# Kernel optimization log

Measured on AMD Instinct MI355X. Metric: run time of the kernel, lower is better.

The kernel has to match this reference:

```python
import jax, jax.numpy as jnp
import numpy as np

B, N, S, D, H = 64, 4096, 8, 256, 512
ITERS = 3
EPS = 1e-8      # slot-attention renormalize epsilon
LN_EPS = 1e-5   # torch LayerNorm default


def _ln(x, g, b):
    m = jnp.mean(x, -1, keepdims=True)
    v = jnp.mean((x - m) ** 2, -1, keepdims=True)
    return (x - m) * jax.lax.rsqrt(v + LN_EPS) * g + b


def setup_inputs() -> dict:
    key = jax.random.key(0)
    ks = jax.random.split(key, 12)

    def xav(k, shape):
        s = (6.0 / (shape[-2] + shape[-1])) ** 0.5
        return jax.random.uniform(k, shape, jnp.float32, -s, s)

    gru_s = 1.0 / (D ** 0.5)
    return {
        "inputs": jax.random.normal(ks[0], (B, N, D), jnp.float32),
        "init_noise": jax.random.normal(ks[1], (B, S, D), jnp.float32),
        "slots_mu": xav(ks[2], (1, 1, D)),
        "slots_log_sigma": xav(ks[3], (1, 1, D)),
        "ln_in_g": jnp.ones(D), "ln_in_b": jnp.zeros(D),
        "ln_slots_g": jnp.ones(D), "ln_slots_b": jnp.zeros(D),
        "ln_mlp_g": jnp.ones(D), "ln_mlp_b": jnp.zeros(D),
        "Wq": xav(ks[4], (D, D)),
        "Wk": xav(ks[5], (D, D)),
        "Wv": xav(ks[6], (D, D)),
        "W_ih": jax.random.uniform(ks[7], (3 * D, D), jnp.float32, -gru_s, gru_s),
        "W_hh": jax.random.uniform(ks[8], (3 * D, D), jnp.float32, -gru_s, gru_s),
        "b_ih": jnp.zeros(3 * D), "b_hh": jnp.zeros(3 * D),
        "W1": xav(ks[9], (H, D)), "b1": jnp.zeros(H),
        "W2": xav(ks[10], (D, H)), "b2": jnp.zeros(D),
    }


def reference(inputs, init_noise, slots_mu, slots_log_sigma,
              ln_in_g, ln_in_b, ln_slots_g, ln_slots_b, ln_mlp_g, ln_mlp_b,
              Wq, Wk, Wv, W_ih, W_hh, b_ih, b_hh, W1, b1, W2, b2):
    x = _ln(inputs, ln_in_g, ln_in_b)               # (B,N,D)
    k = jnp.einsum('bnd,ed->bne', x, Wk)             # (B,N,D)
    v = jnp.einsum('bnd,ed->bne', x, Wv)             # (B,N,D)
    slots = slots_mu + jnp.exp(slots_log_sigma) * init_noise  # (B,S,D)
    scale = D ** (-0.5)
    for _ in range(ITERS):
        prev = slots
        s = _ln(slots, ln_slots_g, ln_slots_b)
        q = jnp.einsum('bsd,ed->bse', s, Wq) * scale
        logits = jnp.einsum('bse,bne->bsn', q, k)    # (B,S,N)
        attn = jax.nn.softmax(logits, -1) + EPS
        attn = attn / jnp.sum(attn, -1, keepdims=True)
        upd = jnp.einsum('bsn,bne->bse', attn, v)    # (B,S,D)
        # GRUCell (torch semantics)
        gx = jnp.einsum('bsd,ed->bse', upd, W_ih) + b_ih
        gh = jnp.einsum('bsd,ed->bse', prev, W_hh) + b_hh
        xr, xz, xn = jnp.split(gx, 3, -1)
        hr, hz, hn = jnp.split(gh, 3, -1)
        r = jax.nn.sigmoid(xr + hr)
        z = jax.nn.sigmoid(xz + hz)
        n = jnp.tanh(xn + r * hn)
        slots = (1.0 - z) * n + z * prev
        # residual MLP
        m = _ln(slots, ln_mlp_g, ln_mlp_b)
        h1 = jax.nn.relu(jnp.einsum('bsd,hd->bsh', m, W1) + b1)
        slots = slots + jnp.einsum('bsh,dh->bsd', h1, W2) + b2
    return slots
```

## Files before the change

kernel.cpp:

```cpp
#include <hip/hip_runtime.h>

#define BB 64
#define NN 4096
#define SS 8
#define DD 256
#define HH 512
#define NCH 8
#define CHK 512
#define LSP 516

typedef __attribute__((ext_vector_type(4))) float f32x4;
typedef __attribute__((ext_vector_type(8))) short short8;
typedef __attribute__((ext_vector_type(8))) __bf16 bf16x8;

static __device__ __forceinline__ f32x4 MFMA(short8 a, short8 b, f32x4 c){
  return __builtin_amdgcn_mfma_f32_16x16x32_bf16(
      __builtin_bit_cast(bf16x8, a), __builtin_bit_cast(bf16x8, b), c, 0, 0, 0);
}

static __device__ __forceinline__ unsigned short f2bf(float f){
  unsigned int x = __builtin_bit_cast(unsigned int, f);
  x += 0x7FFFu + ((x >> 16) & 1u);
  return (unsigned short)(x >> 16);
}

static __device__ __forceinline__ unsigned int pk2(float a, float b){
  return (unsigned int)f2bf(a) | ((unsigned int)f2bf(b) << 16);
}

struct PackDesc {
  const float* src[7];
  unsigned short* dst[7];
  int ET[7];
  int K[7];
  int blkStart[8];
};

__global__ void pack_all_kernel(PackDesc pd){
  int blk = blockIdx.x;
  int seg = 0;
  #pragma unroll
  for(int i = 1; i < 7; ++i) if(blk >= pd.blkStart[i]) seg = i;
  int tid = (blk - pd.blkStart[seg]) * 256 + threadIdx.x;
  int ET = pd.ET[seg], K = pd.K[seg];
  if(tid >= ET * 16 * K) return;
  int i    = tid & 7;
  int lane = (tid >> 3) & 63;
  int rest = tid >> 9;
  int et = rest % ET;
  int kk = rest / ET;
  int row = et * 16 + (lane & 15);
  int col = kk * 32 + ((lane >> 4) << 3) + i;
  pd.dst[seg][tid] = f2bf(pd.src[seg][(size_t)row * K + col]);
}

__global__ __launch_bounds__(256, 2) void proj_kernel(
    const float* __restrict__ inp, const float* __restrict__ g, const float* __restrict__ bta,
    const short8* __restrict__ wkp, const short8* __restrict__ wvp,
    unsigned short* __restrict__ kout, unsigned short* __restrict__ vT)
{
  __shared__ unsigned short xs[64 * 256];
  __shared__ unsigned short vstage[4][1024];
  const int t = threadIdx.x, w = t >> 6, l = t & 63;
  const size_t row0 = (size_t)blockIdx.x * 64;
  const int b = (int)(row0 >> 12);
  const int n_base = (int)(row0 & 4095);
  const int li = l & 15, lg = l >> 4;

  {
    float4 gg[4], bb[4];
    #pragma unroll
    for(int q = 0; q < 4; ++q){
      gg[q] = ((const float4*)g)[li + q * 16];
      bb[q] = ((const float4*)bta)[li + q * 16];
    }
    #pragma unroll
    for(int rr = 0; rr < 4; ++rr){
      int r = w * 16 + rr * 4 + lg;
      const float4* rp = (const float4*)(inp + (row0 + r) * DD);
      float4 x[4];
      #pragma unroll
      for(int q = 0; q < 4; ++q) x[q] = rp[li + q * 16];
      float s1 = 0.f, s2 = 0.f;
      #pragma unroll
      for(int q = 0; q < 4; ++q){
        s1 += x[q].x + x[q].y + x[q].z + x[q].w;
        s2 += x[q].x*x[q].x + x[q].y*x[q].y + x[q].z*x[q].z + x[q].w*x[q].w;
      }
      #pragma unroll
      for(int o = 8; o >= 1; o >>= 1){ s1 += __shfl_xor(s1, o); s2 += __shfl_xor(s2, o); }
      float mean = s1 * (1.0f/256.0f);
      float inv  = rsqrtf(s2 * (1.0f/256.0f) - mean*mean + 1e-5f);
      #pragma unroll
      for(int q = 0; q < 4; ++q){
        float y0 = (x[q].x-mean)*inv*gg[q].x + bb[q].x;
        float y1 = (x[q].y-mean)*inv*gg[q].y + bb[q].y;
        float y2 = (x[q].z-mean)*inv*gg[q].z + bb[q].z;
        float y3 = (x[q].w-mean)*inv*gg[q].w + bb[q].w;
        int byte = r * 512 + ((q * 128 + li * 8) ^ ((r & 7) << 4));
        *(uint2*)((char*)xs + byte) = make_uint2(pk2(y0,y1), pk2(y2,y3));
      }
    }
  }
  __syncthreads();

  const int et0 = w * 4;
  #pragma unroll
  for(int el = 0; el < 4; ++el){
    const int et = et0 + el;
    short8 wb[8];
    #pragma unroll
    for(int kk = 0; kk < 8; ++kk) wb[kk] = wkp[((kk * 16 + et) << 6) + l];
    #pragma unroll
    for(int rg = 0; rg < 4; ++rg){
      const int r = rg * 16 + li;
      f32x4 a = (f32x4){0,0,0,0};
      #pragma unroll
      for(int kk = 0; kk < 8; ++kk){
        int ab = r * 512 + (((kk * 64) + (lg << 4)) ^ ((r & 7) << 4));
        short8 afr = *(const short8*)((const char*)xs + ab);
        a = MFMA(wb[kk], afr, a);
      }
      size_t row = row0 + rg * 16 + li;
      int colb = et * 16 + (lg << 2);
      *(uint2*)(kout + row * DD + colb) = make_uint2(pk2(a[0],a[1]), pk2(a[2],a[3]));
    }
  }
  #pragma unroll
  for(int el = 0; el < 4; ++el){
    const int et = et0 + el;
    short8 wb[8];
    #pragma unroll
    for(int kk = 0; kk < 8; ++kk) wb[kk] = wvp[((kk * 16 + et) << 6) + l];
    char* vs = (char*)&vstage[w][0];
    #pragma unroll
    for(int rg = 0; rg < 4; ++rg){
      const int r = rg * 16 + li;
      f32x4 a = (f32x4){0,0,0,0};
      #pragma unroll
      for(int kk = 0; kk < 8; ++kk){
        int ab = r * 512 + (((kk * 64) + (lg << 4)) ^ ((r & 7) << 4));
        short8 afr = *(const short8*)((const char*)xs + ab);
        a = MFMA(afr, wb[kk], a);
      }
      int nloc = rg * 16 + (lg << 2);
      int byte = li * 128 + ((nloc * 2) ^ ((li & 7) << 4));
      *(uint2*)(vs + byte) = make_uint2(pk2(a[0],a[1]), pk2(a[2],a[3]));
    }
    asm volatile("s_waitcnt lgkmcnt(0)" ::: "memory");
    #pragma unroll
    for(int u = 0; u < 2; ++u){
      int dl = u * 8 + (l >> 3);
      int byte = dl * 128 + (((l & 7) * 16) ^ ((dl & 7) << 4));
      uint4 vv = *(uint4*)(vs + byte);
      int d = et * 16 + dl;
      *(uint4*)(vT + ((size_t)(b * 256 + d) << 12) + n_base + (l & 7) * 8) = vv;
    }
    asm volatile("" ::: "memory");
  }
}

__global__ __launch_bounds__(256, 1) void init_kernel(
    const float* __restrict__ noise, const float* __restrict__ mu, const float* __restrict__ lsg,
    const float* __restrict__ lng, const float* __restrict__ lnb,
    const short8* __restrict__ wqp, float* __restrict__ slots, float* __restrict__ qbuf)
{
  const int b = blockIdx.x, t = threadIdx.x, w = t >> 6, l = t & 63;
  __shared__ float SLN[SS * DD];
  __shared__ unsigned short A1[16 * DD];
  float muv = mu[t];
  float sgv = __expf(lsg[t]);
  #pragma unroll
  for(int s = 0; s < SS; ++s){
    float v = muv + sgv * noise[(size_t)b * 2048 + s * 256 + t];
    slots[(size_t)b * 2048 + s * 256 + t] = v;
    SLN[s * 256 + t] = v;
  }
  __syncthreads();
  float4 g4 = ((const float4*)lng)[l], bb4 = ((const float4*)lnb)[l];
  for(int sh = 0; sh < 2; ++sh){
    int s = w * 2 + sh;
    float4 x4 = ((const float4*)(SLN + s * 256))[l];
    float s1 = x4.x + x4.y + x4.z + x4.w;
    float s2 = x4.x*x4.x + x4.y*x4.y + x4.z*x4.z + x4.w*x4.w;
    #pragma unroll
    for(int o = 32; o >= 1; o >>= 1){ s1 += __shfl_xor(s1, o); s2 += __shfl_xor(s2, o); }
    float mean = s1 * (1.0f/256.0f);
    float inv  = rsqrtf(s2 * (1.0f/256.0f) - mean*mean + 1e-5f);
    float y0 = (x4.x-mean)*inv*g4.x + bb4.x;
    float y1 = (x4.y-mean)*inv*g4.y + bb4.y;
    float y2 = (x4.z-mean)*inv*g4.z + bb4.z;
    float y3 = (x4.w-mean)*inv*g4.w + bb4.w;
    int byte = s * 512 + ((l * 8) ^ ((s & 7) << 4));
    *(uint2*)((char*)A1 + byte) = make_uint2(pk2(y0,y1), pk2(y2,y3));
  }
  __syncthreads();
  const int m = l & 15;
  short8 af[8];
  #pragma unroll
  for(int kk = 0; kk < 8; ++kk){
    int ab = m * 512 + (((kk * 64) + ((l >> 4) << 4)) ^ ((m & 7) << 4));
    af[kk] = *(const short8*)((const char*)A1 + ab);
  }
  #pragma unroll
  for(int i = 0; i < 4; ++i){
    int et = w + i * 4;
    f32x4 c = (f32x4){0,0,0,0};
    #pragma unroll
    for(int kk = 0; kk < 8; ++kk) c = MFMA(af[kk], wqp[((kk * 16 + et) << 6) + l], c);
    int e = et * 16 + (l & 15);
    #pragma unroll
    for(int j = 0; j < 4; ++j){
      int s = ((l >> 4) << 2) + j;
      if(s < 8) qbuf[(size_t)b * 2048 + s * 256 + e] = c[j] * 0.0625f;
    }
  }
}

__global__ __launch_bounds__(256, 3) void attn_kernel(
    const unsigned short* __restrict__ kb_, const unsigned short* __restrict__ vT_,
    const float* __restrict__ qbuf, float* __restrict__ pupd, float* __restrict__ pms)
{
  const int blk = blockIdx.x;
  const int b = blk >> 3, c = blk & 7;
  const int t = threadIdx.x, w = t >> 6, l = t & 63;
  __shared__ float ls[8 * LSP];

  const int m = l & 15;
  short8 aq[8];
  #pragma unroll
  for(int kk = 0; kk < 8; ++kk){
    if(m < 8){
      const float* qp = qbuf + (size_t)b * 2048 + m * 256 + kk * 32 + ((l >> 4) << 3);
      float4 qa = *(const float4*)qp;
      float4 qb = *(const float4*)(qp + 4);
      int4 pv = make_int4((int)pk2(qa.x,qa.y), (int)pk2(qa.z,qa.w),
                          (int)pk2(qb.x,qb.y), (int)pk2(qb.z,qb.w));
      aq[kk] = __builtin_bit_cast(short8, pv);
    } else {
      aq[kk] = (short8){0,0,0,0,0,0,0,0};
    }
  }

  const unsigned short* kb = kb_ + ((size_t)b * NN + (size_t)c * CHK) * DD;
  #pragma unroll
  for(int nt = 0; nt < 8; ++nt){
    int nb = w * 128 + nt * 16;
    f32x4 acc = (f32x4){0,0,0,0};
    #pragma unroll
    for(int kk = 0; kk < 8; ++kk){
      short8 bk = *(const short8*)(kb + (size_t)(nb + m) * DD + kk * 32 + ((l >> 4) << 3));
      acc = MFMA(aq[kk], bk, acc);
    }
    if(l < 32){
      int s4 = (l >> 4) * 4;
      #pragma unroll
      for(int j = 0; j < 4; ++j) ls[(s4 + j) * LSP + nb + m] = acc[j];
    }
  }
  __syncthreads();

  for(int sh = 0; sh < 2; ++sh){
    int s = w * 2 + sh;
    float* base = ls + s * LSP;
    float4 v0 = *(float4*)(base + l * 4);
    float4 v1 = *(float4*)(base + 256 + l * 4);
    float mx = fmaxf(fmaxf(fmaxf(v0.x,v0.y),fmaxf(v0.z,v0.w)),
                     fmaxf(fmaxf(v1.x,v1.y),fmaxf(v1.z,v1.w)));
    #pragma unroll
    for(int o = 32; o >= 1; o >>= 1) mx = fmaxf(mx, __shfl_xor(mx, o));
    float e0 = __expf(v0.x-mx), e1 = __expf(v0.y-mx), e2 = __expf(v0.z-mx), e3 = __expf(v0.w-mx);
    float e4 = __expf(v1.x-mx), e5 = __expf(v1.y-mx), e6 = __expf(v1.z-mx), e7 = __expf(v1.w-mx);
    float sm = e0+e1+e2+e3+e4+e5+e6+e7;
    #pragma unroll
    for(int o = 32; o >= 1; o >>= 1) sm += __shfl_xor(sm, o);
    *(float4*)(base + l * 4)       = make_float4(e0,e1,e2,e3);
    *(float4*)(base + 256 + l * 4) = make_float4(e4,e5,e6,e7);
    if(l == 0){
      pms[(((size_t)b * 8 + c) * 8 + s) * 2    ] = mx;
      pms[(((size_t)b * 8 + c) * 8 + s) * 2 + 1] = sm;
    }
  }
  __syncthreads();

  short8 pa[16];
  #pragma unroll
  for(int kk = 0; kk < 16; ++kk){
    if(m < 8){
      const float* pp = ls + m * LSP + kk * 32 + ((l >> 4) << 3);
      int4 pv = make_int4((int)pk2(pp[0],pp[1]), (int)pk2(pp[2],pp[3]),
                          (int)pk2(pp[4],pp[5]), (int)pk2(pp[6],pp[7]));
      pa[kk] = __builtin_bit_cast(short8, pv);
    } else {
      pa[kk] = (short8){0,0,0,0,0,0,0,0};
    }
  }

  const unsigned short* vt = vT_ + ((size_t)b << 20) + (size_t)c * CHK;
  #pragma unroll
  for(int dt = 0; dt < 4; ++dt){
    int d0 = w * 64 + dt * 16;
    f32x4 acc = (f32x4){0,0,0,0};
    #pragma unroll
    for(int kk = 0; kk < 16; ++kk){
      short8 bv = *(const short8*)(vt + ((size_t)(d0 + m) << 12) + kk * 32 + ((l >> 4) << 3));
      acc = MFMA(pa[kk], bv, acc);
    }
    if(l < 32){
      int s4 = (l >> 4) * 4;
      #pragma unroll
      for(int j = 0; j < 4; ++j)
        pupd[((size_t)b * 8 + c) * 2048 + (s4 + j) * 256 + d0 + m] = acc[j];
    }
  }
}

__global__ __launch_bounds__(512, 1) void update_kernel(
    const float* __restrict__ pupd, const float* __restrict__ pms,
    float* __restrict__ slots, float* __restrict__ qbuf,
    const short8* __restrict__ wih, const short8* __restrict__ whh,
    const float* __restrict__ bih, const float* __restrict__ bhh,
    const short8* __restrict__ w1p, const float* __restrict__ b1v,
    const short8* __restrict__ w2p, const float* __restrict__ b2v,
    const float* __restrict__ lnsg, const float* __restrict__ lnsb,
    const float* __restrict__ lnmg, const float* __restrict__ lnmb,
    const short8* __restrict__ wqp,
    float* __restrict__ dout, const int last)
{
  const int b = blockIdx.x, t = threadIdx.x, w = t >> 6, l = t & 63;
  __shared__ unsigned short A1[16 * 256];
  __shared__ unsigned short A2[16 * 256];
  __shared__ unsigned short A3[16 * 512];
  __shared__ float GR[8 * 256], GZ[8 * 256], GXN[8 * 256], GHN[8 * 256];
  __shared__ float SL[8 * 256];
  __shared__ float PMS[128];

  if(t < 128) PMS[t] = pms[(size_t)b * 128 + t];
  __syncthreads();

  const int col = t & 255, sg = t >> 8;
  float upd[4], pv[4];
  #pragma unroll
  for(int ss = 0; ss < 4; ++ss){
    int s = sg * 4 + ss;
    float mx = -1e30f;
    #pragma unroll
    for(int cc = 0; cc < 8; ++cc) mx = fmaxf(mx, PMS[(cc * 8 + s) * 2]);
    float Z = 0.f, u = 0.f;
    #pragma unroll
    for(int cc = 0; cc < 8; ++cc){
      float e = __expf(PMS[(cc * 8 + s) * 2] - mx);
      Z += e * PMS[(cc * 8 + s) * 2 + 1];
      u += e * pupd[((size_t)b * 8 + cc) * 2048 + s * 256 + col];
    }
    upd[ss] = u / Z;
    pv[ss]  = slots[(size_t)b * 2048 + s * 256 + col];
  }
  #pragma unroll
  for(int ss = 0; ss < 4; ++ss){
    int s = sg * 4 + ss;
    int byte = s * 512 + ((col * 2) ^ ((s & 7) << 4));
    *(unsigned short*)((char*)A1 + byte) = f2bf(upd[ss]);
    *(unsigned short*)((char*)A2 + byte) = f2bf(pv[ss]);
  }
  __syncthreads();

  {
    const int m = l & 15;
    short8 a1f[8], a2f[8];
    #pragma unroll
    for(int kk = 0; kk < 8; ++kk){
      int ab = m * 512 + (((kk * 64) + ((l >> 4) << 4)) ^ ((m & 7) << 4));
      a1f[kk] = *(const short8*)((const char*)A1 + ab);
      a2f[kk] = *(const short8*)((const char*)A2 + ab);
    }
    #pragma unroll
    for(int i = 0; i < 6; ++i){
      int et = w + i * 8;
      f32x4 c1 = (f32x4){0,0,0,0}, c2 = (f32x4){0,0,0,0};
      #pragma unroll
      for(int kk = 0; kk < 8; ++kk){
        c1 = MFMA(a1f[kk], wih[((kk * 48 + et) << 6) + l], c1);
        c2 = MFMA(a2f[kk], whh[((kk * 48 + et) << 6) + l], c2);
      }
      int e = et * 16 + (l & 15);
      float xb = bih[e], hb = bhh[e];
      #pragma unroll
      for(int j = 0; j < 4; ++j){
        int s = ((l >> 4) << 2) + j;
        if(s < 8){
          float x = c1[j] + xb, h = c2[j] + hb;
          if(et < 16)      GR[s * 256 + e      ] = 1.f/(1.f + __expf(-(x + h)));
          else if(et < 32) GZ[s * 256 + (e-256)] = 1.f/(1.f + __expf(-(x + h)));
          else { GXN[s * 256 + (e-512)] = x; GHN[s * 256 + (e-512)] = h; }
        }
      }
    }
  }
  __syncthreads();

  #pragma unroll
  for(int ss = 0; ss < 4; ++ss){
    int s = sg * 4 + ss, idx = s * 256 + col;
    float r = GR[idx], z = GZ[idx], xn = GXN[idx], hn = GHN[idx];
    float nn = tanhf(xn + r * hn);
    SL[idx] = (1.f - z) * nn + z * pv[ss];
  }
  __syncthreads();

  {
    float4 g4 = ((const float4*)lnmg)[l], bb4 = ((const float4*)lnmb)[l];
    int s = w;
    float4 x4 = ((const float4*)(SL + s * 256))[l];
    float s1 = x4.x + x4.y + x4.z + x4.w;
    float s2 = x4.x*x4.x + x4.y*x4.y + x4.z*x4.z + x4.w*x4.w;
    #pragma unroll
    for(int o = 32; o >= 1; o >>= 1){ s1 += __shfl_xor(s1, o); s2 += __shfl_xor(s2, o); }
    float mean = s1 * (1.0f/256.0f);
    float inv  = rsqrtf(s2 * (1.0f/256.0f) - mean*mean + 1e-5f);
    float y0 = (x4.x-mean)*inv*g4.x + bb4.x;
    float y1 = (x4.y-mean)*inv*g4.y + bb4.y;
    float y2 = (x4.z-mean)*inv*g4.z + bb4.z;
    float y3 = (x4.w-mean)*inv*g4.w + bb4.w;
    int byte = s * 512 + ((l * 8) ^ ((s & 7) << 4));
    *(uint2*)((char*)A1 + byte) = make_uint2(pk2(y0,y1), pk2(y2,y3));
  }
  __syncthreads();

  {
    const int m = l & 15;
    short8 af[8];
    #pragma unroll
    for(int kk = 0; kk < 8; ++kk){
      int ab = m * 512 + (((kk * 64) + ((l >> 4) << 4)) ^ ((m & 7) << 4));
      af[kk] = *(const short8*)((const char*)A1 + ab);
    }
    #pragma unroll
    for(int i = 0; i < 4; ++i){
      int et = w + i * 8;
      f32x4 c = (f32x4){0,0,0,0};
      #pragma unroll
      for(int kk = 0; kk < 8; ++kk) c = MFMA(af[kk], w1p[((kk * 32 + et) << 6) + l], c);
      int e = et * 16 + (l & 15);
      float bb = b1v[e];
      #pragma unroll
      for(int j = 0; j < 4; ++j){
        int s = ((l >> 4) << 2) + j;
        if(s < 8){
          float h = fmaxf(c[j] + bb, 0.f);
          int byte = s * 1024 + ((e * 2) ^ ((s & 7) << 4));
          *(unsigned short*)((char*)A3 + byte) = f2bf(h);
        }
      }
    }
  }
  __syncthreads();

  {
    const int m = l & 15;
    short8 af[16];
    #pragma unroll
    for(int kk = 0; kk < 16; ++kk){
      int ab = m * 1024 + (((kk * 64) + ((l >> 4) << 4)) ^ ((m & 7) << 4));
      af[kk] = *(const short8*)((const char*)A3 + ab);
    }
    #pragma unroll
    for(int i = 0; i < 2; ++i){
      int et = w + i * 8;
      f32x4 c = (f32x4){0,0,0,0};
      #pragma unroll
      for(int kk = 0; kk < 16; ++kk) c = MFMA(af[kk], w2p[((kk * 16 + et) << 6) + l], c);
      int e = et * 16 + (l & 15);
      float bb = b2v[e];
      #pragma unroll
      for(int j = 0; j < 4; ++j){
        int s = ((l >> 4) << 2) + j;
        if(s < 8) GR[s * 256 + e] = SL[s * 256 + e] + c[j] + bb;
      }
    }
  }
  __syncthreads();

  for(int i = t; i < 2048; i += 512){
    float v = GR[i];
    slots[(size_t)b * 2048 + i] = v;
    if(last) dout[(size_t)b * 2048 + i] = v;
  }
  {
    float4 g4 = ((const float4*)lnsg)[l], bb4 = ((const float4*)lnsb)[l];
    int s = w;
    float4 x4 = ((const float4*)(GR + s * 256))[l];
    float s1 = x4.x + x4.y + x4.z + x4.w;
    float s2 = x4.x*x4.x + x4.y*x4.y + x4.z*x4.z + x4.w*x4.w;
    #pragma unroll
    for(int o = 32; o >= 1; o >>= 1){ s1 += __shfl_xor(s1, o); s2 += __shfl_xor(s2, o); }
    float mean = s1 * (1.0f/256.0f);
    float inv  = rsqrtf(s2 * (1.0f/256.0f) - mean*mean + 1e-5f);
    float y0 = (x4.x-mean)*inv*g4.x + bb4.x;
    float y1 = (x4.y-mean)*inv*g4.y + bb4.y;
    float y2 = (x4.z-mean)*inv*g4.z + bb4.z;
    float y3 = (x4.w-mean)*inv*g4.w + bb4.w;
    int byte = s * 512 + ((l * 8) ^ ((s & 7) << 4));
    *(uint2*)((char*)A1 + byte) = make_uint2(pk2(y0,y1), pk2(y2,y3));
  }
  __syncthreads();
  {
    const int m = l & 15;
    short8 af[8];
    #pragma unroll
    for(int kk = 0; kk < 8; ++kk){
      int ab = m * 512 + (((kk * 64) + ((l >> 4) << 4)) ^ ((m & 7) << 4));
      af[kk] = *(const short8*)((const char*)A1 + ab);
    }
    #pragma unroll
    for(int i = 0; i < 2; ++i){
      int et = w + i * 8;
      f32x4 c = (f32x4){0,0,0,0};
      #pragma unroll
      for(int kk = 0; kk < 8; ++kk) c = MFMA(af[kk], wqp[((kk * 16 + et) << 6) + l], c);
      int e = et * 16 + (l & 15);
      #pragma unroll
      for(int j = 0; j < 4; ++j){
        int s = ((l >> 4) << 2) + j;
        if(s < 8) qbuf[(size_t)b * 2048 + s * 256 + e] = c[j] * 0.0625f;
      }
    }
  }
}

extern "C" void kernel_launch(void* const* d_in, const int* in_sizes, int n_in,
                              void* d_out, int out_size, void* d_ws, size_t ws_size,
                              hipStream_t stream)
{
  const float* inp   = (const float*)d_in[0];
  const float* noise = (const float*)d_in[1];
  const float* mu    = (const float*)d_in[2];
  const float* lsg   = (const float*)d_in[3];
  const float* lngi  = (const float*)d_in[4];
  const float* lnbi  = (const float*)d_in[5];
  const float* lngs  = (const float*)d_in[6];
  const float* lnbs  = (const float*)d_in[7];
  const float* lngm  = (const float*)d_in[8];
  const float* lnbm  = (const float*)d_in[9];
  const float* Wq    = (const float*)d_in[10];
  const float* Wk    = (const float*)d_in[11];
  const float* Wv    = (const float*)d_in[12];
  const float* Wih   = (const float*)d_in[13];
  const float* Whh   = (const float*)d_in[14];
  const float* bih   = (const float*)d_in[15];
  const float* bhh   = (const float*)d_in[16];
  const float* W1    = (const float*)d_in[17];
  const float* b1    = (const float*)d_in[18];
  const float* W2    = (const float*)d_in[19];
  const float* b2    = (const float*)d_in[20];
  float* dout = (float*)d_out;

  char* ws = (char*)d_ws;
  size_t off = 0;
  unsigned short* kb  = (unsigned short*)(ws + off); off += (size_t)BB*NN*DD*2;
  unsigned short* vT  = (unsigned short*)(ws + off); off += (size_t)BB*NN*DD*2;
  short8* wqp = (short8*)(ws + off); off += (size_t)256*256*2;
  short8* wkp = (short8*)(ws + off); off += (size_t)256*256*2;
  short8* wvp = (short8*)(ws + off); off += (size_t)256*256*2;
  short8* wihp= (short8*)(ws + off); off += (size_t)768*256*2;
  short8* whhp= (short8*)(ws + off); off += (size_t)768*256*2;
  short8* w1p = (short8*)(ws + off); off += (size_t)512*256*2;
  short8* w2p = (short8*)(ws + off); off += (size_t)256*512*2;
  float* qbuf = (float*)(ws + off); off += (size_t)512*256*4;
  float* slots= (float*)(ws + off); off += (size_t)512*256*4;
  float* pupd = (float*)(ws + off); off += (size_t)64*8*8*256*4;
  float* pms  = (float*)(ws + off); off += (size_t)64*8*8*2*4;

  PackDesc pd;
  const float* srcs[7] = {Wq, Wk, Wv, Wih, Whh, W1, W2};
  unsigned short* dsts[7] = {(unsigned short*)wqp, (unsigned short*)wkp, (unsigned short*)wvp,
                             (unsigned short*)wihp, (unsigned short*)whhp,
                             (unsigned short*)w1p, (unsigned short*)w2p};
  int ets[7] = {16, 16, 16, 48, 48, 32, 16};
  int ks [7] = {256, 256, 256, 256, 256, 256, 512};
  int cum = 0;
  for(int i = 0; i < 7; ++i){
    pd.src[i] = srcs[i]; pd.dst[i] = dsts[i]; pd.ET[i] = ets[i]; pd.K[i] = ks[i];
    pd.blkStart[i] = cum;
    cum += (ets[i] * 16 * ks[i] + 255) / 256;
  }
  pd.blkStart[7] = cum;
  pack_all_kernel<<<cum, 256, 0, stream>>>(pd);

  proj_kernel<<<4096, 256, 0, stream>>>(inp, lngi, lnbi, wkp, wvp, kb, vT);
  init_kernel<<<64, 256, 0, stream>>>(noise, mu, lsg, lngs, lnbs, wqp, slots, qbuf);

  for(int it = 0; it < 3; ++it){
    attn_kernel<<<512, 256, 0, stream>>>(kb, vT, qbuf, pupd, pms);
    update_kernel<<<64, 512, 0, stream>>>(pupd, pms, slots, qbuf, wihp, whhp,
        bih, bhh, w1p, b1, w2p, b2, lngs, lnbs, lngm, lnbm, wqp, dout, (it == 2) ? 1 : 0);
  }
}
```

Measured before the change: 422.1 us.

## Split input LayerNorm from K/V projection and widen update kernel to 1024 threads

The fused LayerNorm+projection kernel becomes two kernels. The first writes the normalized input as swizzled bf16 into the K buffer. The second loads that tile directly into LDS with global_load_lds and overwrites it in place with K. This separates the LN latency from the MFMA phase, at the cost of an extra full write and read of the normalized activations through global memory. The per-batch update kernel also doubles its thread count so each wave handles fewer gate, MLP and query output tiles, which shortens its serial latency.

```diff
diff --git a/kernel.cpp b/kernel.cpp
--- a/kernel.cpp
+++ b/kernel.cpp
@@ -26,6 +26,12 @@
 
 static __device__ __forceinline__ unsigned int pk2(float a, float b){
   return (unsigned int)f2bf(a) | ((unsigned int)f2bf(b) << 16);
+}
+
+static __device__ __forceinline__ void gl_lds16(const void* g, void* l){
+  __builtin_amdgcn_global_load_lds(
+      (__attribute__((address_space(1))) const void*)g,
+      (__attribute__((address_space(3))) void*)l, 16, 0, 0);
 }
 
 struct PackDesc {
@@ -54,10 +60,53 @@
   pd.dst[seg][tid] = f2bf(pd.src[seg][(size_t)row * K + col]);
 }
 
-__global__ __launch_bounds__(256, 2) void proj_kernel(
+__global__ __launch_bounds__(256, 4) void ln_kernel(
     const float* __restrict__ inp, const float* __restrict__ g, const float* __restrict__ bta,
+    unsigned short* __restrict__ xln)
+{
+  const int t = threadIdx.x, w = t >> 6, l = t & 63;
+  const size_t row0 = (size_t)blockIdx.x * 64;
+  const int li = l & 15, lg = l >> 4;
+
+  float4 gg[4], bb[4];
+  #pragma unroll
+  for(int q = 0; q < 4; ++q){
+    gg[q] = ((const float4*)g)[li + q * 16];
+    bb[q] = ((const float4*)bta)[li + q * 16];
+  }
+  #pragma unroll
+  for(int rr = 0; rr < 4; ++rr){
+    int r = w * 16 + rr * 4 + lg;
+    const float4* rp = (const float4*)(inp + (row0 + r) * DD);
+    float4 x[4];
+    #pragma unroll
+    for(int q = 0; q < 4; ++q) x[q] = rp[li + q * 16];
+    float s1 = 0.f, s2 = 0.f;
+    #pragma unroll
+    for(int q = 0; q < 4; ++q){
+      s1 += x[q].x + x[q].y + x[q].z + x[q].w;
+      s2 += x[q].x*x[q].x + x[q].y*x[q].y + x[q].z*x[q].z + x[q].w*x[q].w;
+    }
+    #pragma unroll
+    for(int o = 8; o >= 1; o >>= 1){ s1 += __shfl_xor(s1, o); s2 += __shfl_xor(s2, o); }
+    float mean = s1 * (1.0f/256.0f);
+    float inv  = rsqrtf(s2 * (1.0f/256.0f) - mean*mean + 1e-5f);
+    #pragma unroll
+    for(int q = 0; q < 4; ++q){
+      float y0 = (x[q].x-mean)*inv*gg[q].x + bb[q].x;
+      float y1 = (x[q].y-mean)*inv*gg[q].y + bb[q].y;
+      float y2 = (x[q].z-mean)*inv*gg[q].z + bb[q].z;
+      float y3 = (x[q].w-mean)*inv*gg[q].w + bb[q].w;
+      size_t byte = (row0 + r) * 512 + ((q * 128 + li * 8) ^ ((r & 7) << 4));
+      *(uint2*)((char*)xln + byte) = make_uint2(pk2(y0,y1), pk2(y2,y3));
+    }
+  }
+}
+
+__global__ __launch_bounds__(256, 2) void kv_kernel(
+    unsigned short* kb,
     const short8* __restrict__ wkp, const short8* __restrict__ wvp,
-    unsigned short* __restrict__ kout, unsigned short* __restrict__ vT)
+    unsigned short* __restrict__ vT)
 {
   __shared__ unsigned short xs[64 * 256];
   __shared__ unsigned short vstage[4][1024];
@@ -68,40 +117,14 @@
   const int li = l & 15, lg = l >> 4;
 
   {
-    float4 gg[4], bb[4];
-    #pragma unroll
-    for(int q = 0; q < 4; ++q){
-      gg[q] = ((const float4*)g)[li + q * 16];
-      bb[q] = ((const float4*)bta)[li + q * 16];
-    }
-    #pragma unroll
-    for(int rr = 0; rr < 4; ++rr){
-      int r = w * 16 + rr * 4 + lg;
-      const float4* rp = (const float4*)(inp + (row0 + r) * DD);
-      float4 x[4];
-      #pragma unroll
-      for(int q = 0; q < 4; ++q) x[q] = rp[li + q * 16];
-      float s1 = 0.f, s2 = 0.f;
-      #pragma unroll
-      for(int q = 0; q < 4; ++q){
-        s1 += x[q].x + x[q].y + x[q].z + x[q].w;
-        s2 += x[q].x*x[q].x + x[q].y*x[q].y + x[q].z*x[q].z + x[q].w*x[q].w;
-      }
-      #pragma unroll
-      for(int o = 8; o >= 1; o >>= 1){ s1 += __shfl_xor(s1, o); s2 += __shfl_xor(s2, o); }
-      float mean = s1 * (1.0f/256.0f);
-      float inv  = rsqrtf(s2 * (1.0f/256.0f) - mean*mean + 1e-5f);
-      #pragma unroll
-      for(int q = 0; q < 4; ++q){
-        float y0 = (x[q].x-mean)*inv*gg[q].x + bb[q].x;
-        float y1 = (x[q].y-mean)*inv*gg[q].y + bb[q].y;
-        float y2 = (x[q].z-mean)*inv*gg[q].z + bb[q].z;
-        float y3 = (x[q].w-mean)*inv*gg[q].w + bb[q].w;
-        int byte = r * 512 + ((q * 128 + li * 8) ^ ((r & 7) << 4));
-        *(uint2*)((char*)xs + byte) = make_uint2(pk2(y0,y1), pk2(y2,y3));
-      }
-    }
-  }
+    const char* gsrc = (const char*)kb + row0 * 512;
+    #pragma unroll
+    for(int i = 0; i < 8; ++i){
+      int off = w * 8192 + i * 1024;
+      gl_lds16(gsrc + off + l * 16, (char*)xs + off);
+    }
+  }
+  asm volatile("s_waitcnt vmcnt(0)" ::: "memory");
   __syncthreads();
 
   const int et0 = w * 4;
@@ -123,7 +146,7 @@
       }
       size_t row = row0 + rg * 16 + li;
       int colb = et * 16 + (lg << 2);
-      *(uint2*)(kout + row * DD + colb) = make_uint2(pk2(a[0],a[1]), pk2(a[2],a[3]));
+      *(uint2*)(kb + row * DD + colb) = make_uint2(pk2(a[0],a[1]), pk2(a[2],a[3]));
     }
   }
   #pragma unroll
@@ -315,7 +338,7 @@
   }
 }
 
-__global__ __launch_bounds__(512, 1) void update_kernel(
+__global__ __launch_bounds__(1024, 1) void update_kernel(
     const float* __restrict__ pupd, const float* __restrict__ pms,
     float* __restrict__ slots, float* __restrict__ qbuf,
     const short8* __restrict__ wih, const short8* __restrict__ whh,
@@ -339,10 +362,10 @@
   __syncthreads();
 
   const int col = t & 255, sg = t >> 8;
-  float upd[4], pv[4];
-  #pragma unroll
-  for(int ss = 0; ss < 4; ++ss){
-    int s = sg * 4 + ss;
+  float upd[2], pv[2];
+  #pragma unroll
+  for(int ss = 0; ss < 2; ++ss){
+    int s = sg * 2 + ss;
     float mx = -1e30f;
     #pragma unroll
     for(int cc = 0; cc < 8; ++cc) mx = fmaxf(mx, PMS[(cc * 8 + s) * 2]);
@@ -357,8 +380,8 @@
     pv[ss]  = slots[(size_t)b * 2048 + s * 256 + col];
   }
   #pragma unroll
-  for(int ss = 0; ss < 4; ++ss){
-    int s = sg * 4 + ss;
+  for(int ss = 0; ss < 2; ++ss){
+    int s = sg * 2 + ss;
     int byte = s * 512 + ((col * 2) ^ ((s & 7) << 4));
     *(unsigned short*)((char*)A1 + byte) = f2bf(upd[ss]);
     *(unsigned short*)((char*)A2 + byte) = f2bf(pv[ss]);
@@ -375,8 +398,8 @@
       a2f[kk] = *(const short8*)((const char*)A2 + ab);
     }
     #pragma unroll
-    for(int i = 0; i < 6; ++i){
-      int et = w + i * 8;
+    for(int i = 0; i < 3; ++i){
+      int et = w + i * 16;
       f32x4 c1 = (f32x4){0,0,0,0}, c2 = (f32x4){0,0,0,0};
       #pragma unroll
       for(int kk = 0; kk < 8; ++kk){
@@ -390,8 +413,8 @@
         int s = ((l >> 4) << 2) + j;
         if(s < 8){
           float x = c1[j] + xb, h = c2[j] + hb;
-          if(et < 16)      GR[s * 256 + e      ] = 1.f/(1.f + __expf(-(x + h)));
-          else if(et < 32) GZ[s * 256 + (e-256)] = 1.f/(1.f + __expf(-(x + h)));
+          if(i == 0)      GR[s * 256 + e      ] = 1.f/(1.f + __expf(-(x + h)));
+          else if(i == 1) GZ[s * 256 + (e-256)] = 1.f/(1.f + __expf(-(x + h)));
           else { GXN[s * 256 + (e-512)] = x; GHN[s * 256 + (e-512)] = h; }
         }
       }
@@ -400,15 +423,15 @@
   __syncthreads();
 
   #pragma unroll
-  for(int ss = 0; ss < 4; ++ss){
-    int s = sg * 4 + ss, idx = s * 256 + col;
+  for(int ss = 0; ss < 2; ++ss){
+    int s = sg * 2 + ss, idx = s * 256 + col;
     float r = GR[idx], z = GZ[idx], xn = GXN[idx], hn = GHN[idx];
     float nn = tanhf(xn + r * hn);
     SL[idx] = (1.f - z) * nn + z * pv[ss];
   }
   __syncthreads();
 
-  {
+  if(w < 8){
     float4 g4 = ((const float4*)lnmg)[l], bb4 = ((const float4*)lnmb)[l];
     int s = w;
     float4 x4 = ((const float4*)(SL + s * 256))[l];
@@ -436,8 +459,8 @@
       af[kk] = *(const short8*)((const char*)A1 + ab);
     }
     #pragma unroll
-    for(int i = 0; i < 4; ++i){
-      int et = w + i * 8;
+    for(int i = 0; i < 2; ++i){
+      int et = w + i * 16;
       f32x4 c = (f32x4){0,0,0,0};
       #pragma unroll
       for(int kk = 0; kk < 8; ++kk) c = MFMA(af[kk], w1p[((kk * 32 + et) << 6) + l], c);
@@ -464,9 +487,8 @@
       int ab = m * 1024 + (((kk * 64) + ((l >> 4) << 4)) ^ ((m & 7) << 4));
       af[kk] = *(const short8*)((const char*)A3 + ab);
     }
-    #pragma unroll
-    for(int i = 0; i < 2; ++i){
-      int et = w + i * 8;
+    {
+      int et = w;
       f32x4 c = (f32x4){0,0,0,0};
       #pragma unroll
       for(int kk = 0; kk < 16; ++kk) c = MFMA(af[kk], w2p[((kk * 16 + et) << 6) + l], c);
@@ -481,12 +503,12 @@
   }
   __syncthreads();
 
-  for(int i = t; i < 2048; i += 512){
+  for(int i = t; i < 2048; i += 1024){
     float v = GR[i];
     slots[(size_t)b * 2048 + i] = v;
     if(last) dout[(size_t)b * 2048 + i] = v;
   }
-  {
+  if(w < 8){
     float4 g4 = ((const float4*)lnsg)[l], bb4 = ((const float4*)lnsb)[l];
     int s = w;
     float4 x4 = ((const float4*)(GR + s * 256))[l];
@@ -512,9 +534,8 @@
       int ab = m * 512 + (((kk * 64) + ((l >> 4) << 4)) ^ ((m & 7) << 4));
       af[kk] = *(const short8*)((const char*)A1 + ab);
     }
-    #pragma unroll
-    for(int i = 0; i < 2; ++i){
-      int et = w + i * 8;
+    {
+      int et = w;
       f32x4 c = (f32x4){0,0,0,0};
       #pragma unroll
       for(int kk = 0; kk < 8; ++kk) c = MFMA(af[kk], wqp[((kk * 16 + et) << 6) + l], c);
@@ -587,12 +608,13 @@
   pd.blkStart[7] = cum;
   pack_all_kernel<<<cum, 256, 0, stream>>>(pd);
 
-  proj_kernel<<<4096, 256, 0, stream>>>(inp, lngi, lnbi, wkp, wvp, kb, vT);
+  ln_kernel<<<4096, 256, 0, stream>>>(inp, lngi, lnbi, kb);
+  kv_kernel<<<4096, 256, 0, stream>>>(kb, wkp, wvp, vT);
   init_kernel<<<64, 256, 0, stream>>>(noise, mu, lsg, lngs, lnbs, wqp, slots, qbuf);
 
   for(int it = 0; it < 3; ++it){
     attn_kernel<<<512, 256, 0, stream>>>(kb, vT, qbuf, pupd, pms);
-    update_kernel<<<64, 512, 0, stream>>>(pupd, pms, slots, qbuf, wihp, whhp,
+    update_kernel<<<64, 1024, 0, stream>>>(pupd, pms, slots, qbuf, wihp, whhp,
         bih, bhh, w1p, b1, w2p, b2, lngs, lnbs, lngm, lnbm, wqp, dout, (it == 2) ? 1 : 0);
   }
 }
```

After: 485.5 us. 1.15x slower.
